# Optimization experiments

Measured on AMD Instinct MI355X. Metric: run time of the kernel, lower is better.

Reference implementation:

```python
import jax, jax.numpy as jnp
import numpy as np

B, T, C, H = 8, 2048, 1024, 128

def setup_inputs() -> dict:
    key = jax.random.key(0)
    k1, k2, k3, k4 = jax.random.split(key, 4)
    scale = C ** -0.5  # init scale for weights, roughly matches nn.Linear default magnitude
    return {
        "x": jax.random.normal(k1, (B, T, C), dtype=jnp.float32),
        "Wk": jax.random.normal(k2, (C, H), dtype=jnp.float32) * scale,
        "Wq": jax.random.normal(k3, (C, H), dtype=jnp.float32) * scale,
        "Wv": jax.random.normal(k4, (C, H), dtype=jnp.float32) * scale,
    }

def reference(x, Wk, Wq, Wv):
    # x: [B, T, C]; W*: [C, H] (torch Linear weight transposed, bias=False)
    Bx, Tx, Cx = x.shape
    k = x @ Wk  # [B, T, H]
    q = x @ Wq  # [B, T, H]
    v = x @ Wv  # [B, T, H]
    # NOTE: original scales by C**(-0.5) (embedding size), not head_size**-0.5
    scores = jnp.einsum('bth,bsh->bts', q, k) * (Cx ** -0.5)  # [B, T, T]
    causal = jnp.tril(jnp.ones((Tx, Tx), dtype=bool))
    scores = jnp.where(causal, scores, -jnp.inf)
    w = jax.nn.softmax(scores, axis=-1)  # dropout is identity in eval mode
    out = jnp.einsum('bts,bsh->bth', w, v)  # [B, T, H]
    return out
```

## Files before the change

kernel.cpp:

```cpp
#include <hip/hip_runtime.h>


typedef __attribute__((ext_vector_type(8))) short short8;
typedef __attribute__((ext_vector_type(4))) float f32x4;

typedef const __attribute__((address_space(1))) unsigned int* gas_u32p;
typedef __attribute__((address_space(3))) unsigned int* las_u32p;

static __device__ __forceinline__ unsigned short f2bf(float f) {
  unsigned int u = __float_as_uint(f);
  u += 0x7FFF + ((u >> 16) & 1);
  return (unsigned short)(u >> 16);
}

__global__ void wtrans_kernel(const float* __restrict__ Wq,
                              const float* __restrict__ Wk,
                              const float* __restrict__ Wv,
                              unsigned short* __restrict__ Wt) {
  int idx = blockIdx.x * blockDim.x + threadIdx.x;
  int C  = idx >> 3;
  int e  = idx & 7;
  int l  = C & 63;
  int t1 = C >> 6;
  int kh = t1 & 1;
  int t2 = t1 >> 1;
  int w  = t2 % 3;
  int t3 = t2 / 3;
  int wave = t3 & 7;
  int kt   = t3 >> 3;
  int n = wave * 16 + (l & 15);
  int k = kt * 64 + kh * 32 + (l >> 4) * 8 + e;
  const float* W = (w == 0) ? Wq : (w == 1) ? Wk : Wv;
  Wt[idx] = f2bf(W[k * 128 + n]);
}

__global__ __launch_bounds__(512) void qkv_kernel(
    const float* __restrict__ x,
    const unsigned short* __restrict__ Wt,
    unsigned short* __restrict__ q,
    unsigned short* __restrict__ kb,
    unsigned short* __restrict__ vt)
{
  __shared__ float xl[4][4096];
  const int tid  = threadIdx.x;
  const int lane = tid & 63;
  const int wave = tid >> 6;
  const int m0   = blockIdx.x * 64;
  const int lr   = lane & 15;

  f32x4 acc[4][3];
  #pragma unroll
  for (int i = 0; i < 4; ++i)
    #pragma unroll
    for (int w = 0; w < 3; ++w) acc[i][w] = (f32x4){0.f, 0.f, 0.f, 0.f};

  int srow[2], skq[2];
  #pragma unroll
  for (int i = 0; i < 2; ++i) {
    int c  = i * 512 + tid;
    int ln = c & 63;
    int g  = c >> 6;
    srow[i] = (g >> 2) * 16 + (ln & 15);
    skq[i]  = ((g >> 1) & 1) * 8 + (ln >> 4) * 2 + (g & 1);
  }

  #define QSTAGE(KT, BUF)                                                        \
    do {                                                                         \
      _Pragma("unroll")                                                          \
      for (int i = 0; i < 2; ++i) {                                              \
        const float* gsrc = x + (size_t)(m0 + srow[i]) * 1024 + (KT) * 64 + skq[i] * 4; \
        __builtin_amdgcn_global_load_lds((gas_u32p)gsrc,                         \
            (las_u32p)&xl[BUF][(i * 512 + tid) * 4], 16, 0, 0);                  \
      }                                                                          \
    } while (0)

  const unsigned short* w2base = Wt + wave * 3072 + lane * 8;

  #define WLOAD(KT, DST)                                                         \
    do {                                                                         \
      _Pragma("unroll")                                                          \
      for (int w = 0; w < 3; ++w) {                                              \
        DST[w][0] = *reinterpret_cast<const short8*>(w2base + (KT) * 24576 + w * 1024);       \
        DST[w][1] = *reinterpret_cast<const short8*>(w2base + (KT) * 24576 + w * 1024 + 512); \
      }                                                                          \
    } while (0)

  short8 wbuf[2][3][2];

  WLOAD(0, wbuf[0]);
  QSTAGE(0, 0);
  QSTAGE(1, 1);

  #pragma unroll
  for (int kt = 0; kt < 16; ++kt) {
    if (kt < 15) WLOAD(kt + 1, wbuf[(kt + 1) & 1]);
    if (kt < 14) QSTAGE(kt + 2, (kt + 2) & 3);
    if (kt < 14)      asm volatile("s_waitcnt vmcnt(10)" ::: "memory");
    else if (kt < 15) asm volatile("s_waitcnt vmcnt(8)"  ::: "memory");
    else              asm volatile("s_waitcnt vmcnt(0)"  ::: "memory");
    __builtin_amdgcn_sched_barrier(0);
    __builtin_amdgcn_s_barrier();

    short8 af[4][2];
    #pragma unroll
    for (int mf = 0; mf < 4; ++mf)
      #pragma unroll
      for (int kh = 0; kh < 2; ++kh) {
        const float* basep = &xl[kt & 3][((mf * 2 + kh) * 2) * 256 + lane * 4];
        f32x4 h0 = *reinterpret_cast<const f32x4*>(basep);
        f32x4 h1 = *reinterpret_cast<const f32x4*>(basep + 256);
        union { unsigned int w[4]; short8 s; } cv;
        asm("v_cvt_pk_bf16_f32 %0, %1, %2" : "=v"(cv.w[0]) : "v"(h0[0]), "v"(h0[1]));
        asm("v_cvt_pk_bf16_f32 %0, %1, %2" : "=v"(cv.w[1]) : "v"(h0[2]), "v"(h0[3]));
        asm("v_cvt_pk_bf16_f32 %0, %1, %2" : "=v"(cv.w[2]) : "v"(h1[0]), "v"(h1[1]));
        asm("v_cvt_pk_bf16_f32 %0, %1, %2" : "=v"(cv.w[3]) : "v"(h1[2]), "v"(h1[3]));
        af[mf][kh] = cv.s;
      }

    __builtin_amdgcn_s_setprio(1);
    #pragma unroll
    for (int w = 0; w < 3; ++w)
      #pragma unroll
      for (int mf = 0; mf < 4; ++mf) {
        acc[mf][w] = __builtin_amdgcn_mfma_f32_16x16x32_bf16(af[mf][0], wbuf[kt & 1][w][0], acc[mf][w], 0, 0, 0);
        acc[mf][w] = __builtin_amdgcn_mfma_f32_16x16x32_bf16(af[mf][1], wbuf[kt & 1][w][1], acc[mf][w], 0, 0, 0);
      }
    __builtin_amdgcn_s_setprio(0);
  }
  #undef QSTAGE
  #undef WLOAD

  const int h = wave * 16 + lr;
  const int b = m0 >> 11;
  #pragma unroll
  for (int mf = 0; mf < 4; ++mf) {
    int r0 = m0 + mf * 16 + (lane >> 4) * 4;
    #pragma unroll
    for (int j = 0; j < 4; ++j) {
      int r = r0 + j;
      q[(size_t)r * 128 + h] = f2bf(acc[mf][0][j]);
      int rr  = r & 63;
      int nf  = ((rr >> 5) & 1) * 2 + ((rr >> 2) & 1);
      int lrk = ((rr >> 3) & 3) * 4 + (rr & 3);
      size_t kidx = (size_t)(r >> 6) * 8192
                  + (size_t)(((nf * 4 + (h >> 5)) * 64 + ((h >> 3) & 3) * 16 + lrk) * 8 + (h & 7));
      kb[kidx] = f2bf(acc[mf][1][j]);
    }
    int t = r0 & 2047;
    size_t vidx = (size_t)b * 262144 + (size_t)(t >> 6) * 8192
                + (size_t)(((((h >> 4) * 2 + ((t >> 5) & 1)) * 64 + ((t >> 3) & 3) * 16 + (h & 15)) * 8) + (t & 7));
    ushort4 u;
    u.x = f2bf(acc[mf][2][0]); u.y = f2bf(acc[mf][2][1]);
    u.z = f2bf(acc[mf][2][2]); u.w = f2bf(acc[mf][2][3]);
    *reinterpret_cast<ushort4*>(vt + vidx) = u;
  }
}

template<bool MASK>
static __device__ __forceinline__ void body_regs(
    int s, int myrow0, int myrow1, int lg,
    const short8 (&kf)[2][4], const short8 (&vf)[8],
    const short8 (&qf)[2][4], f32x4 (&o)[2][8], float (&lsum)[2])
{
  const float SC = 0.03125f * 1.44269504f;

  f32x4 sT[2][2];
  __builtin_amdgcn_s_setprio(1);
  #pragma unroll
  for (int g = 0; g < 2; ++g)
    #pragma unroll
    for (int nf = 0; nf < 2; ++nf) {
      sT[g][nf] = (f32x4){0.f, 0.f, 0.f, 0.f};
      #pragma unroll
      for (int ks = 0; ks < 4; ++ks)
        sT[g][nf] = __builtin_amdgcn_mfma_f32_16x16x32_bf16(kf[nf][ks], qf[g][ks], sT[g][nf], 0, 0, 0);
    }
  __builtin_amdgcn_s_setprio(0);

  union { unsigned int w[4]; short8 s8; } cv[2];
  #pragma unroll
  for (int g = 0; g < 2; ++g) {
    const int myrow = g ? myrow1 : myrow0;
    float p[8];
    #pragma unroll
    for (int nf = 0; nf < 2; ++nf)
      #pragma unroll
      for (int j = 0; j < 4; ++j) {
        float sv = sT[g][nf][j] * SC;
        if (MASK) {
          int kv = s * 32 + lg * 8 + nf * 4 + j;
          if (kv > myrow) sv = -1e30f;
        }
        p[nf * 4 + j] = exp2f(sv);
      }
    lsum[g] += ((p[0] + p[1]) + (p[2] + p[3])) + ((p[4] + p[5]) + (p[6] + p[7]));
    #pragma unroll
    for (int u = 0; u < 4; ++u)
      asm("v_cvt_pk_bf16_f32 %0, %1, %2" : "=v"(cv[g].w[u]) : "v"(p[u * 2]), "v"(p[u * 2 + 1]));
  }

  __builtin_amdgcn_s_setprio(1);
  #pragma unroll
  for (int g = 0; g < 2; ++g)
    #pragma unroll
    for (int n = 0; n < 8; ++n)
      o[g][n] = __builtin_amdgcn_mfma_f32_16x16x32_bf16(vf[n], cv[g].s8, o[g][n], 0, 0, 0);
  __builtin_amdgcn_s_setprio(0);
}

__global__ __launch_bounds__(256) void attn_kernel(
    const unsigned short* __restrict__ q,
    const unsigned short* __restrict__ kb,
    const unsigned short* __restrict__ vt,
    float* __restrict__ out)
{
  __shared__ unsigned short sb[4][2][2][4096];

  const int tid  = threadIdx.x;
  const int lane = tid & 63;
  const int wv   = tid >> 6;
  const int lr = lane & 15;
  const int lg = lane >> 4;
  const int bid = blockIdx.x;
  const int b  = bid & 7;
  const int g2 = bid >> 3;
  const int tt = (g2 < 32) ? (63 - g2) : (g2 - 32);
  const int t0 = tt * 32;
  const int nb = tt + 1;

  const unsigned short* kbase = kb + (size_t)b * 262144;
  const unsigned short* vbase = vt + (size_t)b * 262144;
  const int myrow0 = t0 + lr;
  const int myrow1 = t0 + 16 + lr;

  short8 qf[2][4];
  #pragma unroll
  for (int g = 0; g < 2; ++g) {
    const unsigned short* qp = q + ((size_t)(b * 2048) + (g ? myrow1 : myrow0)) * 128 + lg * 8;
    #pragma unroll
    for (int ks = 0; ks < 4; ++ks)
      qf[g][ks] = *reinterpret_cast<const short8*>(qp + ks * 32);
  }

  f32x4 o[2][8];
  #pragma unroll
  for (int g = 0; g < 2; ++g)
    #pragma unroll
    for (int n = 0; n < 8; ++n) o[g][n] = (f32x4){0.f, 0.f, 0.f, 0.f};
  float lsum[2] = {0.f, 0.f};

  #define STAGE32(S, BUF)                                                        \
    do {                                                                         \
      const int blk = (S) >> 1, hh = (S) & 1;                                    \
      const unsigned short* kg = kbase + (size_t)blk * 8192 + hh * 4096;         \
      const unsigned short* vg = vbase + (size_t)blk * 8192;                     \
      _Pragma("unroll")                                                          \
      for (int i = 0; i < 8; ++i)                                                \
        __builtin_amdgcn_global_load_lds((gas_u32p)(kg + (i * 64 + lane) * 8),   \
            (las_u32p)&sb[wv][BUF][0][(i * 64 + lane) * 8], 16, 0, 0);           \
      _Pragma("unroll")                                                          \
      for (int i = 0; i < 8; ++i)                                                \
        __builtin_amdgcn_global_load_lds((gas_u32p)(vg + ((i * 2 + hh) * 64 + lane) * 8), \
            (las_u32p)&sb[wv][BUF][1][(i * 64 + lane) * 8], 16, 0, 0);           \
      } while (0)

  #define DSREAD(KF, VF, BUF)                                                    \
    do {                                                                         \
      const unsigned short* klc = sb[wv][BUF][0];                                \
      const unsigned short* vlc = sb[wv][BUF][1];                                \
      _Pragma("unroll")                                                          \
      for (int nf = 0; nf < 2; ++nf)                                             \
        _Pragma("unroll")                                                        \
        for (int ks = 0; ks < 4; ++ks)                                           \
          KF[nf][ks] = *reinterpret_cast<const short8*>(klc + ((nf * 4 + ks) * 64 + lane) * 8); \
      _Pragma("unroll")                                                          \
      for (int n = 0; n < 8; ++n)                                                \
        VF[n] = *reinterpret_cast<const short8*>(vlc + (n * 64 + lane) * 8);     \
    } while (0)

  short8 kfA[2][4], vfA[8], kfB[2][4], vfB[8];

  if (wv < nb)     STAGE32(wv, 0);
  if (wv + 4 < nb) STAGE32(wv + 4, 1);
  if (wv < nb) {
    if (wv + 4 < nb) asm volatile("s_waitcnt vmcnt(16)" ::: "memory");
    else             asm volatile("s_waitcnt vmcnt(0)"  ::: "memory");
    __builtin_amdgcn_sched_barrier(0);
    DSREAD(kfA, vfA, 0);
  }

  #define PHASE(CKF, CVF, NKF, NVF, CBUF, NBUF)                                  \
    do {                                                                         \
      asm volatile("s_waitcnt lgkmcnt(0)" ::: "memory");                         \
      __builtin_amdgcn_sched_barrier(0);                                         \
      if (s + 8 < nb) STAGE32(s + 8, CBUF);                                      \
      if (s + 4 < nb) {                                                          \
        if (s + 8 < nb) asm volatile("s_waitcnt vmcnt(16)" ::: "memory");        \
        else            asm volatile("s_waitcnt vmcnt(0)"  ::: "memory");        \
        __builtin_amdgcn_sched_barrier(0);                                       \
        DSREAD(NKF, NVF, NBUF);                                                  \
      }                                                                          \
      if (s == nb - 1)                                                           \
        body_regs<true >(s, myrow0, myrow1, lg, CKF, CVF, qf, o, lsum);          \
      else                                                                       \
        body_regs<false>(s, myrow0, myrow1, lg, CKF, CVF, qf, o, lsum);          \
    } while (0)

  int s = wv;
  #pragma unroll 1
  while (s < nb) {
    PHASE(kfA, vfA, kfB, vfB, 0, 1);
    s += 4;
    if (s >= nb) break;
    PHASE(kfB, vfB, kfA, vfA, 1, 0);
    s += 4;
  }
  #undef PHASE
  #undef DSREAD
  #undef STAGE32

  __syncthreads();
  float* mb = (float*)&sb[0][0][0][0];
  if (wv != 0) {
    #pragma unroll
    for (int g = 0; g < 2; ++g)
      #pragma unroll
      for (int n = 0; n < 8; ++n) {
        float4 st;
        st.x = o[g][n][0]; st.y = o[g][n][1]; st.z = o[g][n][2]; st.w = o[g][n][3];
        *reinterpret_cast<float4*>(&mb[(size_t)((wv - 1) * 16 + g * 8 + n) * 256 + lane * 4]) = st;
      }
    mb[12288 + (wv - 1) * 128 + lane]      = lsum[0];
    mb[12288 + (wv - 1) * 128 + 64 + lane] = lsum[1];
  }
  __syncthreads();
  if (wv == 0) {
    #pragma unroll
    for (int g = 0; g < 2; ++g) {
      #pragma unroll
      for (int n = 0; n < 8; ++n) {
        #pragma unroll
        for (int w = 1; w < 4; ++w) {
          float4 ad = *reinterpret_cast<const float4*>(
              &mb[(size_t)((w - 1) * 16 + g * 8 + n) * 256 + lane * 4]);
          o[g][n][0] += ad.x; o[g][n][1] += ad.y; o[g][n][2] += ad.z; o[g][n][3] += ad.w;
        }
      }
      float ps = lsum[g];
      #pragma unroll
      for (int w = 1; w < 4; ++w)
        ps += mb[12288 + (w - 1) * 128 + g * 64 + lane];
      ps += __shfl_xor(ps, 16);
      ps += __shfl_xor(ps, 32);
      float rcp = 1.0f / ps;
      float* op = out + ((size_t)(b * 2048) + (g ? myrow1 : myrow0)) * 128;
      #pragma unroll
      for (int n = 0; n < 8; ++n) {
        float4 st;
        st.x = o[g][n][0] * rcp; st.y = o[g][n][1] * rcp;
        st.z = o[g][n][2] * rcp; st.w = o[g][n][3] * rcp;
        *reinterpret_cast<float4*>(op + n * 16 + lg * 4) = st;
      }
    }
  }
}

extern "C" void kernel_launch(void* const* d_in, const int* in_sizes, int n_in,
                              void* d_out, int out_size, void* d_ws, size_t ws_size,
                              hipStream_t stream) {
  const float* x  = (const float*)d_in[0];
  const float* Wk = (const float*)d_in[1];
  const float* Wq = (const float*)d_in[2];
  const float* Wv = (const float*)d_in[3];
  float* out = (float*)d_out;

  char* ws = (char*)d_ws;
  unsigned short* q  = (unsigned short*)(ws);
  unsigned short* kb = (unsigned short*)(ws + (4u  << 20));
  unsigned short* vt = (unsigned short*)(ws + (8u  << 20));
  unsigned short* Wt = (unsigned short*)(ws + (12u << 20));

  wtrans_kernel<<<dim3(1536), dim3(256), 0, stream>>>(Wq, Wk, Wv, Wt);
  qkv_kernel<<<dim3(256), dim3(512), 0, stream>>>(x, Wt, q, kb, vt);
  attn_kernel<<<dim3(512), dim3(256), 0, stream>>>(q, kb, vt, out);
}
```

Before: 60.03 us.

## Load K/V fragments directly from global into registers, drop LDS staging

The LDS double-buffered staging of K and V tiles (global_load_lds followed by ds_read) is replaced by direct global loads into register fragments. K for the next step is prefetched one iteration ahead and V is loaded at the start of each phase. Shared memory shrinks to just the final reduction buffer, and launch bounds now request two blocks per CU, aiming for higher occupancy and fewer LDS round trips. The risk is exposed global-load latency, since V is loaded just before use and its prefetch depth is reduced, plus register pressure from the occupancy bound.

After: 57.54 us. 4.1% less time.

```diff
diff --git a/kernel.cpp b/kernel.cpp
--- a/kernel.cpp
+++ b/kernel.cpp
@@ -208,13 +208,13 @@
   __builtin_amdgcn_s_setprio(0);
 }
 
-__global__ __launch_bounds__(256) void attn_kernel(
+__global__ __launch_bounds__(256, 2) void attn_kernel(
     const unsigned short* __restrict__ q,
     const unsigned short* __restrict__ kb,
     const unsigned short* __restrict__ vt,
     float* __restrict__ out)
 {
-  __shared__ unsigned short sb[4][2][2][4096];
+  __shared__ float mb[12672];
 
   const int tid  = threadIdx.x;
   const int lane = tid & 63;
@@ -249,78 +249,53 @@
     for (int n = 0; n < 8; ++n) o[g][n] = (f32x4){0.f, 0.f, 0.f, 0.f};
   float lsum[2] = {0.f, 0.f};
 
-  #define STAGE32(S, BUF)                                                        \
-    do {                                                                         \
-      const int blk = (S) >> 1, hh = (S) & 1;                                    \
-      const unsigned short* kg = kbase + (size_t)blk * 8192 + hh * 4096;         \
-      const unsigned short* vg = vbase + (size_t)blk * 8192;                     \
-      _Pragma("unroll")                                                          \
-      for (int i = 0; i < 8; ++i)                                                \
-        __builtin_amdgcn_global_load_lds((gas_u32p)(kg + (i * 64 + lane) * 8),   \
-            (las_u32p)&sb[wv][BUF][0][(i * 64 + lane) * 8], 16, 0, 0);           \
-      _Pragma("unroll")                                                          \
-      for (int i = 0; i < 8; ++i)                                                \
-        __builtin_amdgcn_global_load_lds((gas_u32p)(vg + ((i * 2 + hh) * 64 + lane) * 8), \
-            (las_u32p)&sb[wv][BUF][1][(i * 64 + lane) * 8], 16, 0, 0);           \
-      } while (0)
-
-  #define DSREAD(KF, VF, BUF)                                                    \
-    do {                                                                         \
-      const unsigned short* klc = sb[wv][BUF][0];                                \
-      const unsigned short* vlc = sb[wv][BUF][1];                                \
+  #define GLOADK(KF, S)                                                          \
+    do {                                                                         \
+      const unsigned short* kg = kbase + (size_t)((S) >> 1) * 8192 + ((S) & 1) * 4096; \
       _Pragma("unroll")                                                          \
       for (int nf = 0; nf < 2; ++nf)                                             \
         _Pragma("unroll")                                                        \
         for (int ks = 0; ks < 4; ++ks)                                           \
-          KF[nf][ks] = *reinterpret_cast<const short8*>(klc + ((nf * 4 + ks) * 64 + lane) * 8); \
+          KF[nf][ks] = *reinterpret_cast<const short8*>(kg + ((nf * 4 + ks) * 64 + lane) * 8); \
+    } while (0)
+
+  #define GLOADV(S)                                                              \
+    do {                                                                         \
+      const unsigned short* vg = vbase + (size_t)((S) >> 1) * 8192;              \
+      const int hh = (S) & 1;                                                    \
       _Pragma("unroll")                                                          \
       for (int n = 0; n < 8; ++n)                                                \
-        VF[n] = *reinterpret_cast<const short8*>(vlc + (n * 64 + lane) * 8);     \
-    } while (0)
-
-  short8 kfA[2][4], vfA[8], kfB[2][4], vfB[8];
-
-  if (wv < nb)     STAGE32(wv, 0);
-  if (wv + 4 < nb) STAGE32(wv + 4, 1);
-  if (wv < nb) {
-    if (wv + 4 < nb) asm volatile("s_waitcnt vmcnt(16)" ::: "memory");
-    else             asm volatile("s_waitcnt vmcnt(0)"  ::: "memory");
-    __builtin_amdgcn_sched_barrier(0);
-    DSREAD(kfA, vfA, 0);
-  }
-
-  #define PHASE(CKF, CVF, NKF, NVF, CBUF, NBUF)                                  \
-    do {                                                                         \
-      asm volatile("s_waitcnt lgkmcnt(0)" ::: "memory");                         \
-      __builtin_amdgcn_sched_barrier(0);                                         \
-      if (s + 8 < nb) STAGE32(s + 8, CBUF);                                      \
-      if (s + 4 < nb) {                                                          \
-        if (s + 8 < nb) asm volatile("s_waitcnt vmcnt(16)" ::: "memory");        \
-        else            asm volatile("s_waitcnt vmcnt(0)"  ::: "memory");        \
-        __builtin_amdgcn_sched_barrier(0);                                       \
-        DSREAD(NKF, NVF, NBUF);                                                  \
-      }                                                                          \
+        vf[n] = *reinterpret_cast<const short8*>(vg + ((n * 2 + hh) * 64 + lane) * 8); \
+    } while (0)
+
+  short8 kfA[2][4], kfB[2][4], vf[8];
+
+  if (wv < nb) GLOADK(kfA, wv);
+
+  #define PHASE(CURK, NXTK)                                                      \
+    do {                                                                         \
+      GLOADV(s);                                                                 \
+      if (s + 4 < nb) GLOADK(NXTK, s + 4);                                       \
       if (s == nb - 1)                                                           \
-        body_regs<true >(s, myrow0, myrow1, lg, CKF, CVF, qf, o, lsum);          \
+        body_regs<true >(s, myrow0, myrow1, lg, CURK, vf, qf, o, lsum);          \
       else                                                                       \
-        body_regs<false>(s, myrow0, myrow1, lg, CKF, CVF, qf, o, lsum);          \
+        body_regs<false>(s, myrow0, myrow1, lg, CURK, vf, qf, o, lsum);          \
     } while (0)
 
   int s = wv;
   #pragma unroll 1
   while (s < nb) {
-    PHASE(kfA, vfA, kfB, vfB, 0, 1);
+    PHASE(kfA, kfB);
     s += 4;
     if (s >= nb) break;
-    PHASE(kfB, vfB, kfA, vfA, 1, 0);
+    PHASE(kfB, kfA);
     s += 4;
   }
   #undef PHASE
-  #undef DSREAD
-  #undef STAGE32
+  #undef GLOADK
+  #undef GLOADV
 
   __syncthreads();
-  float* mb = (float*)&sb[0][0][0][0];
   if (wv != 0) {
     #pragma unroll
     for (int g = 0; g < 2; ++g)
```
